# Performance work log

Measured on AMD Instinct MI355X. Metric: run time of the kernel, lower is better.

Reference implementation:

```python
import jax, jax.numpy as jnp
import numpy as np

VOCAB = 100000
EMB = 256
HID = 512
HDIR = HID // 2
T = 10            # tagset size
START = 8
STOP = 9
S = 4096          # sequence length
NEG = -10000.0


def setup_inputs() -> dict:
    key = jax.random.key(0)
    ks = jax.random.split(key, 16)
    sentence = jax.random.randint(ks[0], (S,), 0, VOCAB)
    emb = jax.random.normal(ks[1], (VOCAB, EMB), dtype=jnp.float32) * 0.02
    s = 1.0 / np.sqrt(HDIR).astype(np.float32)

    def lstm_weights(k):
        k1, k2, k3, k4 = jax.random.split(k, 4)
        return (
            jax.random.uniform(k1, (4 * HDIR, EMB), jnp.float32, -s, s),
            jax.random.uniform(k2, (4 * HDIR, HDIR), jnp.float32, -s, s),
            jax.random.uniform(k3, (4 * HDIR,), jnp.float32, -s, s),
            jax.random.uniform(k4, (4 * HDIR,), jnp.float32, -s, s),
        )

    Wih_f, Whh_f, bih_f, bhh_f = lstm_weights(ks[2])
    Wih_b, Whh_b, bih_b, bhh_b = lstm_weights(ks[3])
    so = 1.0 / np.sqrt(HID).astype(np.float32)
    W_out = jax.random.uniform(ks[4], (T, HID), jnp.float32, -so, so)
    b_out = jax.random.uniform(ks[5], (T,), jnp.float32, -so, so)
    transitions = jax.random.normal(ks[6], (T, T), dtype=jnp.float32)
    transitions = transitions.at[START, :].set(NEG).at[:, STOP].set(NEG)
    return {
        "sentence": sentence, "emb": emb,
        "Wih_f": Wih_f, "Whh_f": Whh_f, "bih_f": bih_f, "bhh_f": bhh_f,
        "Wih_b": Wih_b, "Whh_b": Whh_b, "bih_b": bih_b, "bhh_b": bhh_b,
        "W_out": W_out, "b_out": b_out, "transitions": transitions,
    }


def _lstm_dir(x, Wih, Whh, bih, bhh):
    # x: [S, EMB] -> hidden states [S, HDIR]; PyTorch gate order i,f,g,o
    b = bih + bhh
    xW = x @ Wih.T + b  # precompute input contribution: [S, 4*HDIR]

    def step(carry, xw_t):
        h, c = carry
        z = xw_t + Whh @ h
        i, f, g, o = jnp.split(z, 4)
        i = jax.nn.sigmoid(i); f = jax.nn.sigmoid(f)
        g = jnp.tanh(g); o = jax.nn.sigmoid(o)
        c = f * c + i * g
        h = o * jnp.tanh(c)
        return (h, c), h

    h0 = jnp.zeros((HDIR,), x.dtype)
    _, hs = jax.lax.scan(step, (h0, h0), xW)
    return hs


def _viterbi(feats, transitions):
    # feats: [S, T]
    def vstep(fv, feat):
        ntv = fv[None, :] + transitions        # [T(next), T(prev)]
        bp = jnp.argmax(ntv, axis=1)           # [T]
        fv_new = jnp.max(ntv, axis=1) + feat   # [T]
        return fv_new, bp

    init = jnp.full((T,), NEG, feats.dtype).at[START].set(0.0)
    fv, bps = jax.lax.scan(vstep, init, feats)
    terminal = fv + transitions[STOP]
    best = jnp.argmax(terminal)
    score = terminal[best]

    def back(tag, bp):
        return bp[tag], tag

    _, path_rev = jax.lax.scan(back, best, bps[::-1])
    return score, path_rev[::-1]


def reference(sentence, emb, Wih_f, Whh_f, bih_f, bhh_f,
              Wih_b, Whh_b, bih_b, bhh_b, W_out, b_out, transitions):
    x = emb[sentence]                                   # [S, EMB]
    h_f = _lstm_dir(x, Wih_f, Whh_f, bih_f, bhh_f)      # [S, HDIR]
    h_b = _lstm_dir(x[::-1], Wih_b, Whh_b, bih_b, bhh_b)[::-1]
    lstm_out = jnp.concatenate([h_f, h_b], axis=-1)     # [S, HID]
    feats = lstm_out @ W_out.T + b_out                  # [S, T]
    score, path = _viterbi(feats, transitions)
    return score, path
```

## Files before the change

### kernel.cpp

```cpp
#include <hip/hip_runtime.h>
#include <math.h>

#define S_LEN 4096
#define HDIRC 256
#define NTAG 10
#define START_TAG 8
#define STOP_TAG 9
#define NEGV -10000.0f

#define XW_OFF 0UL
#define XW_SZ  (2UL * S_LEN * 1024)
#define HS_OFF (XW_OFF + XW_SZ)
#define HS_SZ  (2UL * S_LEN * 256)
#define WT_OFF (HS_OFF + HS_SZ)
#define WT_SZ  (2UL * 256 * 1024)
#define FE_OFF (WT_OFF + WT_SZ)
#define FE_SZ  ((size_t)S_LEN * NTAG)
#define RING_OFF (FE_OFF + FE_SZ)
#define RING_SZ (2UL * 2 * 256 * 2)

__global__ void transpose_wih(const float* __restrict__ wf,
                              const float* __restrict__ wb,
                              float* __restrict__ wT) {
    __shared__ float tile[32][33];
    const float* src = blockIdx.z ? wb : wf;
    float* dst = wT + (size_t)blockIdx.z * 256 * 1024;
    int x = blockIdx.x * 32 + threadIdx.x;
    int y = blockIdx.y * 32 + threadIdx.y;
    tile[threadIdx.y][threadIdx.x] = src[y * 256 + x];
    __syncthreads();
    int ko = blockIdx.x * 32 + threadIdx.y;
    int ro = blockIdx.y * 32 + threadIdx.x;
    dst[(size_t)ko * 1024 + ro] = tile[threadIdx.x][threadIdx.y];
}

__global__ __launch_bounds__(256) void xw_gemm(
    const int* __restrict__ sent, const float* __restrict__ emb,
    const float* __restrict__ wT,
    const float* __restrict__ bih_f, const float* __restrict__ bhh_f,
    const float* __restrict__ bih_b, const float* __restrict__ bhh_b,
    float* __restrict__ xw) {
    int dir = blockIdx.y;
    int t0 = blockIdx.x * 8;
    int tid = threadIdx.x;
    __shared__ __align__(16) float xs[8][256];
    for (int i = 0; i < 8; ++i) {
        int t = t0 + i;
        int pos = dir ? (S_LEN - 1 - t) : t;
        int idx = sent[pos];
        xs[i][tid] = emb[(size_t)idx * 256 + tid];
    }
    __syncthreads();
    const float* w = wT + (size_t)dir * 256 * 1024;
    const float* bi = dir ? bih_b : bih_f;
    const float* bh = dir ? bhh_b : bhh_f;
    float4 bv;
    bv.x = bi[4 * tid + 0] + bh[4 * tid + 0];
    bv.y = bi[4 * tid + 1] + bh[4 * tid + 1];
    bv.z = bi[4 * tid + 2] + bh[4 * tid + 2];
    bv.w = bi[4 * tid + 3] + bh[4 * tid + 3];
    float4 acc[8];
#pragma unroll
    for (int i = 0; i < 8; ++i) acc[i] = bv;
    for (int k4 = 0; k4 < 64; ++k4) {
        float4 w0 = ((const float4*)(w + (size_t)(4 * k4 + 0) * 1024))[tid];
        float4 w1 = ((const float4*)(w + (size_t)(4 * k4 + 1) * 1024))[tid];
        float4 w2 = ((const float4*)(w + (size_t)(4 * k4 + 2) * 1024))[tid];
        float4 w3 = ((const float4*)(w + (size_t)(4 * k4 + 3) * 1024))[tid];
#pragma unroll
        for (int i = 0; i < 8; ++i) {
            float4 xv = *(const float4*)&xs[i][4 * k4];
            acc[i].x = fmaf(w0.x, xv.x, acc[i].x);
            acc[i].y = fmaf(w0.y, xv.x, acc[i].y);
            acc[i].z = fmaf(w0.z, xv.x, acc[i].z);
            acc[i].w = fmaf(w0.w, xv.x, acc[i].w);
            acc[i].x = fmaf(w1.x, xv.y, acc[i].x);
            acc[i].y = fmaf(w1.y, xv.y, acc[i].y);
            acc[i].z = fmaf(w1.z, xv.y, acc[i].z);
            acc[i].w = fmaf(w1.w, xv.y, acc[i].w);
            acc[i].x = fmaf(w2.x, xv.z, acc[i].x);
            acc[i].y = fmaf(w2.y, xv.z, acc[i].y);
            acc[i].z = fmaf(w2.z, xv.z, acc[i].z);
            acc[i].w = fmaf(w2.w, xv.z, acc[i].w);
            acc[i].x = fmaf(w3.x, xv.w, acc[i].x);
            acc[i].y = fmaf(w3.y, xv.w, acc[i].y);
            acc[i].z = fmaf(w3.z, xv.w, acc[i].z);
            acc[i].w = fmaf(w3.w, xv.w, acc[i].w);
        }
    }
#pragma unroll
    for (int i = 0; i < 8; ++i)
        ((float4*)(xw + ((size_t)dir * S_LEN + t0 + i) * 1024))[tid] = acc[i];
}

__global__ __launch_bounds__(256, 1) void lstm_rec(
    const float* __restrict__ whh_f, const float* __restrict__ whh_b,
    const float* __restrict__ xw, float* __restrict__ hs,
    unsigned long long* __restrict__ ring) {
    int blk = blockIdx.x;
    int dir = blk >> 4;
    int b = blk & 15;
    int tid = threadIdx.x;
    int g = tid >> 6;
    int lane = tid & 63;
    int v = lane >> 2;
    int u = lane & 3;

    __shared__ __align__(16) float wl[16384];
    __shared__ __align__(16) float hbf[320];
    __shared__ __align__(16) float actb[64];
    float4* wl4 = (float4*)wl;

    const float* whh = dir ? whh_b : whh_f;
#pragma unroll
    for (int j = 0; j < 4; ++j)
#pragma unroll
        for (int i = 0; i < 4; ++i)
            wl4[((g * 16 + j * 4 + i) << 6) + lane] =
                *(const float4*)(whh +
                    (size_t)(g * 256 + b * 16 + 4 * u + j) * 256 + 16 * v + 4 * i);

    const float* xwd = xw + (size_t)dir * S_LEN * 1024;
    float* hsd = hs + (size_t)dir * S_LEN * 256;
    unsigned long long* ringd = ring + dir * 512;

    for (int i = tid; i < 320; i += 256) hbf[i] = 0.f;
    __syncthreads();

    float4 w00 = wl4[((g * 16 + 0) << 6) + lane];
    float4 w01 = wl4[((g * 16 + 1) << 6) + lane];
    float4 w02 = wl4[((g * 16 + 2) << 6) + lane];
    float4 w03 = wl4[((g * 16 + 3) << 6) + lane];
    float4 w10 = wl4[((g * 16 + 4) << 6) + lane];
    float4 w11 = wl4[((g * 16 + 5) << 6) + lane];
    float4 w12 = wl4[((g * 16 + 6) << 6) + lane];
    float4 w13 = wl4[((g * 16 + 7) << 6) + lane];
    float4 w20 = wl4[((g * 16 + 8) << 6) + lane];
    float4 w21 = wl4[((g * 16 + 9) << 6) + lane];
    float4 w22 = wl4[((g * 16 + 10) << 6) + lane];
    float4 w23 = wl4[((g * 16 + 11) << 6) + lane];
    float4 w30 = wl4[((g * 16 + 12) << 6) + lane];
    float4 w31 = wl4[((g * 16 + 13) << 6) + lane];
    float4 w32 = wl4[((g * 16 + 14) << 6) + lane];
    float4 w33 = wl4[((g * 16 + 15) << 6) + lane];

    float c = 0.f;
    int crow = g * 256 + b * 16 + (lane & 15);
    float xw_cur = (lane < 16) ? xwd[crow] : 0.f;
    int sel = lane & 3;

    for (int t = 0; t < S_LEN; ++t) {
        const float4* hb4 = (const float4*)hbf + v * 5;
        float4 h0 = hb4[0], h1 = hb4[1], h2 = hb4[2], h3 = hb4[3];
        float4 a0, a1, a2, a3;
        a0.x = w00.x * h0.x; a0.y = w00.y * h0.y; a0.z = w00.z * h0.z; a0.w = w00.w * h0.w;
        a1.x = w10.x * h0.x; a1.y = w10.y * h0.y; a1.z = w10.z * h0.z; a1.w = w10.w * h0.w;
        a2.x = w20.x * h0.x; a2.y = w20.y * h0.y; a2.z = w20.z * h0.z; a2.w = w20.w * h0.w;
        a3.x = w30.x * h0.x; a3.y = w30.y * h0.y; a3.z = w30.z * h0.z; a3.w = w30.w * h0.w;

        a0.x = fmaf(w01.x, h1.x, a0.x); a0.y = fmaf(w01.y, h1.y, a0.y);
        a0.z = fmaf(w01.z, h1.z, a0.z); a0.w = fmaf(w01.w, h1.w, a0.w);
        a1.x = fmaf(w11.x, h1.x, a1.x); a1.y = fmaf(w11.y, h1.y, a1.y);
        a1.z = fmaf(w11.z, h1.z, a1.z); a1.w = fmaf(w11.w, h1.w, a1.w);
        a2.x = fmaf(w21.x, h1.x, a2.x); a2.y = fmaf(w21.y, h1.y, a2.y);
        a2.z = fmaf(w21.z, h1.z, a2.z); a2.w = fmaf(w21.w, h1.w, a2.w);
        a3.x = fmaf(w31.x, h1.x, a3.x); a3.y = fmaf(w31.y, h1.y, a3.y);
        a3.z = fmaf(w31.z, h1.z, a3.z); a3.w = fmaf(w31.w, h1.w, a3.w);

        a0.x = fmaf(w02.x, h2.x, a0.x); a0.y = fmaf(w02.y, h2.y, a0.y);
        a0.z = fmaf(w02.z, h2.z, a0.z); a0.w = fmaf(w02.w, h2.w, a0.w);
        a1.x = fmaf(w12.x, h2.x, a1.x); a1.y = fmaf(w12.y, h2.y, a1.y);
        a1.z = fmaf(w12.z, h2.z, a1.z); a1.w = fmaf(w12.w, h2.w, a1.w);
        a2.x = fmaf(w22.x, h2.x, a2.x); a2.y = fmaf(w22.y, h2.y, a2.y);
        a2.z = fmaf(w22.z, h2.z, a2.z); a2.w = fmaf(w22.w, h2.w, a2.w);
        a3.x = fmaf(w32.x, h2.x, a3.x); a3.y = fmaf(w32.y, h2.y, a3.y);
        a3.z = fmaf(w32.z, h2.z, a3.z); a3.w = fmaf(w32.w, h2.w, a3.w);

        a0.x = fmaf(w03.x, h3.x, a0.x); a0.y = fmaf(w03.y, h3.y, a0.y);
        a0.z = fmaf(w03.z, h3.z, a0.z); a0.w = fmaf(w03.w, h3.w, a0.w);
        a1.x = fmaf(w13.x, h3.x, a1.x); a1.y = fmaf(w13.y, h3.y, a1.y);
        a1.z = fmaf(w13.z, h3.z, a1.z); a1.w = fmaf(w13.w, h3.w, a1.w);
        a2.x = fmaf(w23.x, h3.x, a2.x); a2.y = fmaf(w23.y, h3.y, a2.y);
        a2.z = fmaf(w23.z, h3.z, a2.z); a2.w = fmaf(w23.w, h3.w, a2.w);
        a3.x = fmaf(w33.x, h3.x, a3.x); a3.y = fmaf(w33.y, h3.y, a3.y);
        a3.z = fmaf(w33.z, h3.z, a3.z); a3.w = fmaf(w33.w, h3.w, a3.w);

        float s0 = (a0.x + a0.y) + (a0.z + a0.w);
        float s1 = (a1.x + a1.y) + (a1.z + a1.w);
        float s2 = (a2.x + a2.y) + (a2.z + a2.w);
        float s3 = (a3.x + a3.y) + (a3.z + a3.w);

#pragma unroll
        for (int off = 4; off < 64; off <<= 1) {
            s0 += __shfl_xor(s0, off, 64);
            s1 += __shfl_xor(s1, off, 64);
            s2 += __shfl_xor(s2, off, 64);
            s3 += __shfl_xor(s3, off, 64);
        }
        int srcl = lane >> 2;
        float t0v = __shfl(s0, srcl, 64);
        float t1v = __shfl(s1, srcl, 64);
        float t2v = __shfl(s2, srcl, 64);
        float t3v = __shfl(s3, srcl, 64);
        float ss = (sel == 0) ? t0v : (sel == 1) ? t1v : (sel == 2) ? t2v : t3v;

        int tn = (t + 1 < S_LEN) ? t + 1 : t;
        float xw_next = 0.f;
        if (lane < 16) {
            float z = xw_cur + ss;
            float act = (g == 2) ? tanhf(z) : 1.f / (1.f + expf(-z));
            actb[(lane & 15) * 4 + g] = act;
            xw_next = xwd[(size_t)tn * 1024 + crow];
        }
        __syncthreads();

        if (g == 0) {
            unsigned long long* slot = ringd + (size_t)(t & 1) * 256;
            unsigned int want = (unsigned int)(t + 1);
            if (lane < 16) {
                float4 A = *(const float4*)&actb[lane * 4];
                c = fmaf(A.y, c, A.x * A.z);
                float h = A.w * tanhf(c);
                hsd[(size_t)t * 256 + b * 16 + lane] = h;
                unsigned long long pk = ((unsigned long long)want << 32) |
                                        (unsigned long long)__float_as_uint(h);
                __hip_atomic_store(&slot[b * 16 + lane], pk,
                                   __ATOMIC_RELAXED, __HIP_MEMORY_SCOPE_AGENT);
            }
            unsigned long long v0, v1, v2, v3;
            for (;;) {
                v0 = __hip_atomic_load(&slot[lane], __ATOMIC_RELAXED, __HIP_MEMORY_SCOPE_AGENT);
                v1 = __hip_atomic_load(&slot[lane + 64], __ATOMIC_RELAXED, __HIP_MEMORY_SCOPE_AGENT);
                v2 = __hip_atomic_load(&slot[lane + 128], __ATOMIC_RELAXED, __HIP_MEMORY_SCOPE_AGENT);
                v3 = __hip_atomic_load(&slot[lane + 192], __ATOMIC_RELAXED, __HIP_MEMORY_SCOPE_AGENT);
                bool ok = ((unsigned int)(v0 >> 32) == want) &
                          ((unsigned int)(v1 >> 32) == want) &
                          ((unsigned int)(v2 >> 32) == want) &
                          ((unsigned int)(v3 >> 32) == want);
                if (__all(ok)) break;
            }
            int sl = lane & 15, ch = lane >> 4;
            hbf[(ch + 0) * 20 + sl]  = __uint_as_float((unsigned int)v0);
            hbf[(ch + 4) * 20 + sl]  = __uint_as_float((unsigned int)v1);
            hbf[(ch + 8) * 20 + sl]  = __uint_as_float((unsigned int)v2);
            hbf[(ch + 12) * 20 + sl] = __uint_as_float((unsigned int)v3);
        }
        xw_cur = xw_next;
        __syncthreads();
    }
}

__global__ __launch_bounds__(64) void feats_k(const float* __restrict__ hs,
                                              const float* __restrict__ wout,
                                              const float* __restrict__ bout,
                                              float* __restrict__ feats) {
    int t = blockIdx.x, tau = blockIdx.y, lane = threadIdx.x;
    const float* hf = hs + (size_t)t * 256;
    const float* hbk = hs + (size_t)S_LEN * 256 + (size_t)(S_LEN - 1 - t) * 256;
    const float* w = wout + (size_t)tau * 512;
    float s = 0.f;
#pragma unroll
    for (int m = 0; m < 4; ++m) s = fmaf(w[lane + 64 * m], hf[lane + 64 * m], s);
#pragma unroll
    for (int m = 0; m < 4; ++m) s = fmaf(w[256 + lane + 64 * m], hbk[lane + 64 * m], s);
#pragma unroll
    for (int off = 32; off > 0; off >>= 1) s += __shfl_down(s, off, 64);
    if (lane == 0) feats[(size_t)t * NTAG + tau] = s + bout[tau];
}

__global__ __launch_bounds__(64) void viterbi_k(const float* __restrict__ feats,
                                                const float* __restrict__ trans,
                                                float* __restrict__ out) {
    __shared__ float fstage[128 * NTAG];
    __shared__ unsigned char bp[S_LEN * NTAG];
    __shared__ float path[S_LEN];
    __shared__ float term[16];
    int tid = threadIdx.x;
    int rr = (tid < NTAG) ? tid : 0;
    float tr[NTAG];
#pragma unroll
    for (int j = 0; j < NTAG; ++j) tr[j] = trans[rr * NTAG + j];
    float trstop = trans[STOP_TAG * NTAG + rr];
    float fv = (tid == START_TAG) ? 0.f : NEGV;

    for (int t0 = 0; t0 < S_LEN; t0 += 128) {
        __syncthreads();
        for (int i = tid; i < 128 * NTAG; i += 64) fstage[i] = feats[(size_t)t0 * NTAG + i];
        __syncthreads();
        for (int tt = 0; tt < 128; ++tt) {
            float b0 = __shfl(fv, 0, 64), b1 = __shfl(fv, 1, 64);
            float b2 = __shfl(fv, 2, 64), b3 = __shfl(fv, 3, 64);
            float b4 = __shfl(fv, 4, 64), b5 = __shfl(fv, 5, 64);
            float b6 = __shfl(fv, 6, 64), b7 = __shfl(fv, 7, 64);
            float b8 = __shfl(fv, 8, 64), b9 = __shfl(fv, 9, 64);
            float best = b0 + tr[0]; int bj = 0;
            float vv;
            vv = b1 + tr[1]; if (vv > best) { best = vv; bj = 1; }
            vv = b2 + tr[2]; if (vv > best) { best = vv; bj = 2; }
            vv = b3 + tr[3]; if (vv > best) { best = vv; bj = 3; }
            vv = b4 + tr[4]; if (vv > best) { best = vv; bj = 4; }
            vv = b5 + tr[5]; if (vv > best) { best = vv; bj = 5; }
            vv = b6 + tr[6]; if (vv > best) { best = vv; bj = 6; }
            vv = b7 + tr[7]; if (vv > best) { best = vv; bj = 7; }
            vv = b8 + tr[8]; if (vv > best) { best = vv; bj = 8; }
            vv = b9 + tr[9]; if (vv > best) { best = vv; bj = 9; }
            if (tid < NTAG) {
                bp[(t0 + tt) * NTAG + tid] = (unsigned char)bj;
                fv = best + fstage[tt * NTAG + tid];
            }
        }
    }
    if (tid < NTAG) term[tid] = fv + trstop;
    __syncthreads();
    if (tid == 0) {
        float best = -3.4e38f; int bi = 0;
#pragma unroll
        for (int i = 0; i < NTAG; ++i) {
            float v = term[i];
            if (v > best) { best = v; bi = i; }
        }
        out[0] = best;
        int tag = bi;
        for (int t = S_LEN - 1; t >= 0; --t) {
            path[t] = (float)tag;
            tag = bp[t * NTAG + tag];
        }
    }
    __syncthreads();
    for (int i = tid; i < S_LEN; i += 64) out[1 + i] = path[i];
}

extern "C" void kernel_launch(void* const* d_in, const int* in_sizes, int n_in,
                              void* d_out, int out_size, void* d_ws, size_t ws_size,
                              hipStream_t stream) {
    const int* sent = (const int*)d_in[0];
    const float* emb = (const float*)d_in[1];
    const float* wih_f = (const float*)d_in[2];
    const float* whh_f = (const float*)d_in[3];
    const float* bih_f = (const float*)d_in[4];
    const float* bhh_f = (const float*)d_in[5];
    const float* wih_b = (const float*)d_in[6];
    const float* whh_b = (const float*)d_in[7];
    const float* bih_b = (const float*)d_in[8];
    const float* bhh_b = (const float*)d_in[9];
    const float* wout = (const float*)d_in[10];
    const float* bout = (const float*)d_in[11];
    const float* trans = (const float*)d_in[12];

    float* ws = (float*)d_ws;
    float* xw = ws + XW_OFF;
    float* hs = ws + HS_OFF;
    float* wT = ws + WT_OFF;
    float* fe = ws + FE_OFF;
    unsigned long long* ring = (unsigned long long*)(ws + RING_OFF);

    hipLaunchKernelGGL(transpose_wih, dim3(8, 32, 2), dim3(32, 32), 0, stream,
                       wih_f, wih_b, wT);
    hipLaunchKernelGGL(xw_gemm, dim3(S_LEN / 8, 2), dim3(256), 0, stream,
                       sent, emb, wT, bih_f, bhh_f, bih_b, bhh_b, xw);
    hipLaunchKernelGGL(lstm_rec, dim3(32), dim3(256), 0, stream,
                       whh_f, whh_b, xw, hs, ring);
    hipLaunchKernelGGL(feats_k, dim3(S_LEN, NTAG), dim3(64), 0, stream,
                       hs, wout, bout, fe);
    hipLaunchKernelGGL(viterbi_k, dim3(1), dim3(64), 0, stream,
                       fe, trans, (float*)d_out);
}
```

Baseline: 8.145 ms.

## Remove block barriers from LSTM recurrence by having each wave own full gate sets

Each wavefront in the recurrent kernel now computes all four gates for four hidden units, so gate activations and the cell update stay inside the wave and are exchanged with shuffles. The shared-memory activation buffer and both per-step __syncthreads are gone, and every wave polls the global ring itself, then redistributes h with shuffles. Weights are now read from LDS every step instead of being held in registers. This removes intra-block synchronization from the serial critical path, at the cost of extra LDS traffic and four times as many waves polling global memory each step.

```diff
diff --git a/kernel.cpp b/kernel.cpp
--- a/kernel.cpp
+++ b/kernel.cpp
@@ -101,89 +101,85 @@
     int dir = blk >> 4;
     int b = blk & 15;
     int tid = threadIdx.x;
-    int g = tid >> 6;
+    int w = tid >> 6;
     int lane = tid & 63;
     int v = lane >> 2;
     int u = lane & 3;
-
-    __shared__ __align__(16) float wl[16384];
-    __shared__ __align__(16) float hbf[320];
-    __shared__ __align__(16) float actb[64];
-    float4* wl4 = (float4*)wl;
+    int D0 = b * 16 + w * 4;
+
+    __shared__ __align__(16) float4 wl4[4096];
 
     const float* whh = dir ? whh_b : whh_f;
 #pragma unroll
     for (int j = 0; j < 4; ++j)
 #pragma unroll
         for (int i = 0; i < 4; ++i)
-            wl4[((g * 16 + j * 4 + i) << 6) + lane] =
-                *(const float4*)(whh +
-                    (size_t)(g * 256 + b * 16 + 4 * u + j) * 256 + 16 * v + 4 * i);
+            wl4[((w * 16 + j * 4 + i) << 6) + lane] =
+                *(const float4*)(whh + (size_t)(u * 256 + D0 + j) * 256 + 16 * v + 4 * i);
+    __syncthreads();
 
     const float* xwd = xw + (size_t)dir * S_LEN * 1024;
     float* hsd = hs + (size_t)dir * S_LEN * 256;
     unsigned long long* ringd = ring + dir * 512;
 
-    for (int i = tid; i < 320; i += 256) hbf[i] = 0.f;
-    __syncthreads();
-
-    float4 w00 = wl4[((g * 16 + 0) << 6) + lane];
-    float4 w01 = wl4[((g * 16 + 1) << 6) + lane];
-    float4 w02 = wl4[((g * 16 + 2) << 6) + lane];
-    float4 w03 = wl4[((g * 16 + 3) << 6) + lane];
-    float4 w10 = wl4[((g * 16 + 4) << 6) + lane];
-    float4 w11 = wl4[((g * 16 + 5) << 6) + lane];
-    float4 w12 = wl4[((g * 16 + 6) << 6) + lane];
-    float4 w13 = wl4[((g * 16 + 7) << 6) + lane];
-    float4 w20 = wl4[((g * 16 + 8) << 6) + lane];
-    float4 w21 = wl4[((g * 16 + 9) << 6) + lane];
-    float4 w22 = wl4[((g * 16 + 10) << 6) + lane];
-    float4 w23 = wl4[((g * 16 + 11) << 6) + lane];
-    float4 w30 = wl4[((g * 16 + 12) << 6) + lane];
-    float4 w31 = wl4[((g * 16 + 13) << 6) + lane];
-    float4 w32 = wl4[((g * 16 + 14) << 6) + lane];
-    float4 w33 = wl4[((g * 16 + 15) << 6) + lane];
-
-    float c = 0.f;
-    int crow = g * 256 + b * 16 + (lane & 15);
-    float xw_cur = (lane < 16) ? xwd[crow] : 0.f;
-    int sel = lane & 3;
+    float4 hc0 = make_float4(0.f, 0.f, 0.f, 0.f);
+    float4 hc1 = hc0, hc2 = hc0, hc3 = hc0;
+    float c0 = 0.f, c1 = 0.f, c2 = 0.f, c3 = 0.f;
+    float4 xwv = *(const float4*)(xwd + u * 256 + D0);
+    int base = lane & ~3;
+    int pb = 4 * lane;
+
+#define WSLOT(j, i) wl4[((w * 16 + (j)*4 + (i)) << 6) + lane]
 
     for (int t = 0; t < S_LEN; ++t) {
-        const float4* hb4 = (const float4*)hbf + v * 5;
-        float4 h0 = hb4[0], h1 = hb4[1], h2 = hb4[2], h3 = hb4[3];
-        float4 a0, a1, a2, a3;
-        a0.x = w00.x * h0.x; a0.y = w00.y * h0.y; a0.z = w00.z * h0.z; a0.w = w00.w * h0.w;
-        a1.x = w10.x * h0.x; a1.y = w10.y * h0.y; a1.z = w10.z * h0.z; a1.w = w10.w * h0.w;
-        a2.x = w20.x * h0.x; a2.y = w20.y * h0.y; a2.z = w20.z * h0.z; a2.w = w20.w * h0.w;
-        a3.x = w30.x * h0.x; a3.y = w30.y * h0.y; a3.z = w30.z * h0.z; a3.w = w30.w * h0.w;
-
-        a0.x = fmaf(w01.x, h1.x, a0.x); a0.y = fmaf(w01.y, h1.y, a0.y);
-        a0.z = fmaf(w01.z, h1.z, a0.z); a0.w = fmaf(w01.w, h1.w, a0.w);
-        a1.x = fmaf(w11.x, h1.x, a1.x); a1.y = fmaf(w11.y, h1.y, a1.y);
-        a1.z = fmaf(w11.z, h1.z, a1.z); a1.w = fmaf(w11.w, h1.w, a1.w);
-        a2.x = fmaf(w21.x, h1.x, a2.x); a2.y = fmaf(w21.y, h1.y, a2.y);
-        a2.z = fmaf(w21.z, h1.z, a2.z); a2.w = fmaf(w21.w, h1.w, a2.w);
-        a3.x = fmaf(w31.x, h1.x, a3.x); a3.y = fmaf(w31.y, h1.y, a3.y);
-        a3.z = fmaf(w31.z, h1.z, a3.z); a3.w = fmaf(w31.w, h1.w, a3.w);
-
-        a0.x = fmaf(w02.x, h2.x, a0.x); a0.y = fmaf(w02.y, h2.y, a0.y);
-        a0.z = fmaf(w02.z, h2.z, a0.z); a0.w = fmaf(w02.w, h2.w, a0.w);
-        a1.x = fmaf(w12.x, h2.x, a1.x); a1.y = fmaf(w12.y, h2.y, a1.y);
-        a1.z = fmaf(w12.z, h2.z, a1.z); a1.w = fmaf(w12.w, h2.w, a1.w);
-        a2.x = fmaf(w22.x, h2.x, a2.x); a2.y = fmaf(w22.y, h2.y, a2.y);
-        a2.z = fmaf(w22.z, h2.z, a2.z); a2.w = fmaf(w22.w, h2.w, a2.w);
-        a3.x = fmaf(w32.x, h2.x, a3.x); a3.y = fmaf(w32.y, h2.y, a3.y);
-        a3.z = fmaf(w32.z, h2.z, a3.z); a3.w = fmaf(w32.w, h2.w, a3.w);
-
-        a0.x = fmaf(w03.x, h3.x, a0.x); a0.y = fmaf(w03.y, h3.y, a0.y);
-        a0.z = fmaf(w03.z, h3.z, a0.z); a0.w = fmaf(w03.w, h3.w, a0.w);
-        a1.x = fmaf(w13.x, h3.x, a1.x); a1.y = fmaf(w13.y, h3.y, a1.y);
-        a1.z = fmaf(w13.z, h3.z, a1.z); a1.w = fmaf(w13.w, h3.w, a1.w);
-        a2.x = fmaf(w23.x, h3.x, a2.x); a2.y = fmaf(w23.y, h3.y, a2.y);
-        a2.z = fmaf(w23.z, h3.z, a2.z); a2.w = fmaf(w23.w, h3.w, a2.w);
-        a3.x = fmaf(w33.x, h3.x, a3.x); a3.y = fmaf(w33.y, h3.y, a3.y);
-        a3.z = fmaf(w33.z, h3.z, a3.z); a3.w = fmaf(w33.w, h3.w, a3.w);
+        float4 q, a0, a1, a2, a3;
+        q = WSLOT(0, 0);
+        a0.x = q.x * hc0.x; a0.y = q.y * hc0.y; a0.z = q.z * hc0.z; a0.w = q.w * hc0.w;
+        q = WSLOT(1, 0);
+        a1.x = q.x * hc0.x; a1.y = q.y * hc0.y; a1.z = q.z * hc0.z; a1.w = q.w * hc0.w;
+        q = WSLOT(2, 0);
+        a2.x = q.x * hc0.x; a2.y = q.y * hc0.y; a2.z = q.z * hc0.z; a2.w = q.w * hc0.w;
+        q = WSLOT(3, 0);
+        a3.x = q.x * hc0.x; a3.y = q.y * hc0.y; a3.z = q.z * hc0.z; a3.w = q.w * hc0.w;
+
+        q = WSLOT(0, 1);
+        a0.x = fmaf(q.x, hc1.x, a0.x); a0.y = fmaf(q.y, hc1.y, a0.y);
+        a0.z = fmaf(q.z, hc1.z, a0.z); a0.w = fmaf(q.w, hc1.w, a0.w);
+        q = WSLOT(1, 1);
+        a1.x = fmaf(q.x, hc1.x, a1.x); a1.y = fmaf(q.y, hc1.y, a1.y);
+        a1.z = fmaf(q.z, hc1.z, a1.z); a1.w = fmaf(q.w, hc1.w, a1.w);
+        q = WSLOT(2, 1);
+        a2.x = fmaf(q.x, hc1.x, a2.x); a2.y = fmaf(q.y, hc1.y, a2.y);
+        a2.z = fmaf(q.z, hc1.z, a2.z); a2.w = fmaf(q.w, hc1.w, a2.w);
+        q = WSLOT(3, 1);
+        a3.x = fmaf(q.x, hc1.x, a3.x); a3.y = fmaf(q.y, hc1.y, a3.y);
+        a3.z = fmaf(q.z, hc1.z, a3.z); a3.w = fmaf(q.w, hc1.w, a3.w);
+
+        q = WSLOT(0, 2);
+        a0.x = fmaf(q.x, hc2.x, a0.x); a0.y = fmaf(q.y, hc2.y, a0.y);
+        a0.z = fmaf(q.z, hc2.z, a0.z); a0.w = fmaf(q.w, hc2.w, a0.w);
+        q = WSLOT(1, 2);
+        a1.x = fmaf(q.x, hc2.x, a1.x); a1.y = fmaf(q.y, hc2.y, a1.y);
+        a1.z = fmaf(q.z, hc2.z, a1.z); a1.w = fmaf(q.w, hc2.w, a1.w);
+        q = WSLOT(2, 2);
+        a2.x = fmaf(q.x, hc2.x, a2.x); a2.y = fmaf(q.y, hc2.y, a2.y);
+        a2.z = fmaf(q.z, hc2.z, a2.z); a2.w = fmaf(q.w, hc2.w, a2.w);
+        q = WSLOT(3, 2);
+        a3.x = fmaf(q.x, hc2.x, a3.x); a3.y = fmaf(q.y, hc2.y, a3.y);
+        a3.z = fmaf(q.z, hc2.z, a3.z); a3.w = fmaf(q.w, hc2.w, a3.w);
+
+        q = WSLOT(0, 3);
+        a0.x = fmaf(q.x, hc3.x, a0.x); a0.y = fmaf(q.y, hc3.y, a0.y);
+        a0.z = fmaf(q.z, hc3.z, a0.z); a0.w = fmaf(q.w, hc3.w, a0.w);
+        q = WSLOT(1, 3);
+        a1.x = fmaf(q.x, hc3.x, a1.x); a1.y = fmaf(q.y, hc3.y, a1.y);
+        a1.z = fmaf(q.z, hc3.z, a1.z); a1.w = fmaf(q.w, hc3.w, a1.w);
+        q = WSLOT(2, 3);
+        a2.x = fmaf(q.x, hc3.x, a2.x); a2.y = fmaf(q.y, hc3.y, a2.y);
+        a2.z = fmaf(q.z, hc3.z, a2.z); a2.w = fmaf(q.w, hc3.w, a2.w);
+        q = WSLOT(3, 3);
+        a3.x = fmaf(q.x, hc3.x, a3.x); a3.y = fmaf(q.y, hc3.y, a3.y);
+        a3.z = fmaf(q.z, hc3.z, a3.z); a3.w = fmaf(q.w, hc3.w, a3.w);
 
         float s0 = (a0.x + a0.y) + (a0.z + a0.w);
         float s1 = (a1.x + a1.y) + (a1.z + a1.w);
@@ -197,57 +193,75 @@
             s2 += __shfl_xor(s2, off, 64);
             s3 += __shfl_xor(s3, off, 64);
         }
-        int srcl = lane >> 2;
-        float t0v = __shfl(s0, srcl, 64);
-        float t1v = __shfl(s1, srcl, 64);
-        float t2v = __shfl(s2, srcl, 64);
-        float t3v = __shfl(s3, srcl, 64);
-        float ss = (sel == 0) ? t0v : (sel == 1) ? t1v : (sel == 2) ? t2v : t3v;
+
+        float z0 = s0 + xwv.x, z1 = s1 + xwv.y, z2 = s2 + xwv.z, z3 = s3 + xwv.w;
+        float e0, e1, e2, e3;
+        if (u == 2) {
+            e0 = tanhf(z0); e1 = tanhf(z1); e2 = tanhf(z2); e3 = tanhf(z3);
+        } else {
+            e0 = 1.f / (1.f + expf(-z0)); e1 = 1.f / (1.f + expf(-z1));
+            e2 = 1.f / (1.f + expf(-z2)); e3 = 1.f / (1.f + expf(-z3));
+        }
 
         int tn = (t + 1 < S_LEN) ? t + 1 : t;
-        float xw_next = 0.f;
-        if (lane < 16) {
-            float z = xw_cur + ss;
-            float act = (g == 2) ? tanhf(z) : 1.f / (1.f + expf(-z));
-            actb[(lane & 15) * 4 + g] = act;
-            xw_next = xwd[(size_t)tn * 1024 + crow];
-        }
-        __syncthreads();
-
-        if (g == 0) {
-            unsigned long long* slot = ringd + (size_t)(t & 1) * 256;
-            unsigned int want = (unsigned int)(t + 1);
-            if (lane < 16) {
-                float4 A = *(const float4*)&actb[lane * 4];
-                c = fmaf(A.y, c, A.x * A.z);
-                float h = A.w * tanhf(c);
-                hsd[(size_t)t * 256 + b * 16 + lane] = h;
-                unsigned long long pk = ((unsigned long long)want << 32) |
-                                        (unsigned long long)__float_as_uint(h);
-                __hip_atomic_store(&slot[b * 16 + lane], pk,
-                                   __ATOMIC_RELAXED, __HIP_MEMORY_SCOPE_AGENT);
-            }
-            unsigned long long v0, v1, v2, v3;
-            for (;;) {
-                v0 = __hip_atomic_load(&slot[lane], __ATOMIC_RELAXED, __HIP_MEMORY_SCOPE_AGENT);
-                v1 = __hip_atomic_load(&slot[lane + 64], __ATOMIC_RELAXED, __HIP_MEMORY_SCOPE_AGENT);
-                v2 = __hip_atomic_load(&slot[lane + 128], __ATOMIC_RELAXED, __HIP_MEMORY_SCOPE_AGENT);
-                v3 = __hip_atomic_load(&slot[lane + 192], __ATOMIC_RELAXED, __HIP_MEMORY_SCOPE_AGENT);
-                bool ok = ((unsigned int)(v0 >> 32) == want) &
-                          ((unsigned int)(v1 >> 32) == want) &
-                          ((unsigned int)(v2 >> 32) == want) &
-                          ((unsigned int)(v3 >> 32) == want);
-                if (__all(ok)) break;
-            }
-            int sl = lane & 15, ch = lane >> 4;
-            hbf[(ch + 0) * 20 + sl]  = __uint_as_float((unsigned int)v0);
-            hbf[(ch + 4) * 20 + sl]  = __uint_as_float((unsigned int)v1);
-            hbf[(ch + 8) * 20 + sl]  = __uint_as_float((unsigned int)v2);
-            hbf[(ch + 12) * 20 + sl] = __uint_as_float((unsigned int)v3);
-        }
-        xw_cur = xw_next;
-        __syncthreads();
-    }
+        float4 xwn = *(const float4*)(xwd + (size_t)tn * 1024 + u * 256 + D0);
+
+        float i0 = __shfl(e0, base + 0, 64), f0 = __shfl(e0, base + 1, 64);
+        float g0 = __shfl(e0, base + 2, 64), o0 = __shfl(e0, base + 3, 64);
+        float i1 = __shfl(e1, base + 0, 64), f1 = __shfl(e1, base + 1, 64);
+        float g1 = __shfl(e1, base + 2, 64), o1 = __shfl(e1, base + 3, 64);
+        float i2 = __shfl(e2, base + 0, 64), f2 = __shfl(e2, base + 1, 64);
+        float g2 = __shfl(e2, base + 2, 64), o2 = __shfl(e2, base + 3, 64);
+        float i3 = __shfl(e3, base + 0, 64), f3 = __shfl(e3, base + 1, 64);
+        float g3 = __shfl(e3, base + 2, 64), o3 = __shfl(e3, base + 3, 64);
+        c0 = fmaf(f0, c0, i0 * g0); float h0v = o0 * tanhf(c0);
+        c1 = fmaf(f1, c1, i1 * g1); float h1v = o1 * tanhf(c1);
+        c2 = fmaf(f2, c2, i2 * g2); float h2v = o2 * tanhf(c2);
+        c3 = fmaf(f3, c3, i3 * g3); float h3v = o3 * tanhf(c3);
+
+        unsigned long long* slot = ringd + (size_t)(t & 1) * 256;
+        unsigned int want = (unsigned int)(t + 1);
+        if (lane == 0) {
+            *(float4*)(hsd + (size_t)t * 256 + D0) = make_float4(h0v, h1v, h2v, h3v);
+            unsigned long long hw = ((unsigned long long)want << 32);
+            __hip_atomic_store(&slot[D0 + 0], hw | __float_as_uint(h0v),
+                               __ATOMIC_RELAXED, __HIP_MEMORY_SCOPE_AGENT);
+            __hip_atomic_store(&slot[D0 + 1], hw | __float_as_uint(h1v),
+                               __ATOMIC_RELAXED, __HIP_MEMORY_SCOPE_AGENT);
+            __hip_atomic_store(&slot[D0 + 2], hw | __float_as_uint(h2v),
+                               __ATOMIC_RELAXED, __HIP_MEMORY_SCOPE_AGENT);
+            __hip_atomic_store(&slot[D0 + 3], hw | __float_as_uint(h3v),
+                               __ATOMIC_RELAXED, __HIP_MEMORY_SCOPE_AGENT);
+        }
+
+        unsigned long long p0, p1, p2, p3;
+        for (;;) {
+            p0 = __hip_atomic_load(&slot[pb + 0], __ATOMIC_RELAXED, __HIP_MEMORY_SCOPE_AGENT);
+            p1 = __hip_atomic_load(&slot[pb + 1], __ATOMIC_RELAXED, __HIP_MEMORY_SCOPE_AGENT);
+            p2 = __hip_atomic_load(&slot[pb + 2], __ATOMIC_RELAXED, __HIP_MEMORY_SCOPE_AGENT);
+            p3 = __hip_atomic_load(&slot[pb + 3], __ATOMIC_RELAXED, __HIP_MEMORY_SCOPE_AGENT);
+            bool ok = ((unsigned int)(p0 >> 32) == want) &
+                      ((unsigned int)(p1 >> 32) == want) &
+                      ((unsigned int)(p2 >> 32) == want) &
+                      ((unsigned int)(p3 >> 32) == want);
+            if (__all(ok)) break;
+        }
+        float m0 = __uint_as_float((unsigned int)p0);
+        float m1 = __uint_as_float((unsigned int)p1);
+        float m2 = __uint_as_float((unsigned int)p2);
+        float m3 = __uint_as_float((unsigned int)p3);
+
+        hc0.x = __shfl(m0, base + 0, 64); hc0.y = __shfl(m1, base + 0, 64);
+        hc0.z = __shfl(m2, base + 0, 64); hc0.w = __shfl(m3, base + 0, 64);
+        hc1.x = __shfl(m0, base + 1, 64); hc1.y = __shfl(m1, base + 1, 64);
+        hc1.z = __shfl(m2, base + 1, 64); hc1.w = __shfl(m3, base + 1, 64);
+        hc2.x = __shfl(m0, base + 2, 64); hc2.y = __shfl(m1, base + 2, 64);
+        hc2.z = __shfl(m2, base + 2, 64); hc2.w = __shfl(m3, base + 2, 64);
+        hc3.x = __shfl(m0, base + 3, 64); hc3.y = __shfl(m1, base + 3, 64);
+        hc3.z = __shfl(m2, base + 3, 64); hc3.w = __shfl(m3, base + 3, 64);
+        xwv = xwn;
+    }
+#undef WSLOT
 }
 
 __global__ __launch_bounds__(64) void feats_k(const float* __restrict__ hs,
```

New measurement: 23.82 ms. 2.92x slower.
